# Performance work log

Measured on AMD Instinct MI355X. Metric: run time of the kernel, lower is better.

Reference implementation:

```python
import jax, jax.numpy as jnp
import numpy as np

LAMBDA_POS = 0.5
LAMBDA_RAD = 0.5
LAMBDA_UNPAIR = 0.5
EPS = 1e-6
N_PRED = 20


def setup_inputs() -> dict:
    key = jax.random.key(0)
    k1, k2 = jax.random.split(key)
    B, L = 1000000, 12
    pred = jax.random.uniform(k1, (B, N_PRED, 4), dtype=jnp.float32)
    label = jax.random.uniform(k2, (B, L, 4), dtype=jnp.float32)
    return {"pred": pred, "label": label}


def reference(pred, label):
    # pred: [B, 20, 4] (x, y, radius, prob); label: [B, L, 4]
    B, L = label.shape[0], label.shape[1]
    yl = label[:, :, None, :]   # [B, L, 1, 4]
    yp = pred[:, None, :, :]    # [B, 1, 20, 4]
    dist = jnp.sqrt((yl[..., 0] - yp[..., 0]) ** 2 + (yl[..., 1] - yp[..., 1]) ** 2)  # [B, L, 20]
    rdiff = jnp.abs(yl[..., 2] - yp[..., 2])  # [B, L, 20]
    cost = LAMBDA_POS * dist + LAMBDA_RAD * rdiff  # [B, L, 20]
    idx = jnp.argmin(cost, axis=-1)  # [B, L]

    matched = jnp.take_along_axis(pred, idx[:, :, None], axis=1)  # [B, L, 4]
    mdist = jnp.sqrt((label[..., 0] - matched[..., 0]) ** 2 + (label[..., 1] - matched[..., 1]) ** 2)
    mrdiff = jnp.abs(label[..., 2] - matched[..., 2])
    prob_pair = -jnp.log(matched[..., 3] + EPS)  # prob_loss(p, 1)
    loss_pair = jnp.sum(LAMBDA_POS * mdist + LAMBDA_RAD * mrdiff + prob_pair, axis=-1)  # [B]

    # pair_mask[i] = 1 if any label matched pred i
    mask = jnp.zeros((B, N_PRED), dtype=pred.dtype)
    mask = mask.at[jnp.arange(B)[:, None], idx].set(1.0)

    unpair_term = (-jnp.log(1.0 - pred[..., 3] + EPS) + LAMBDA_RAD * pred[..., 2]) * LAMBDA_UNPAIR  # [B, 20]
    loss_unpair = jnp.sum((1.0 - mask) * unpair_term, axis=-1)  # [B]

    return loss_pair / L + loss_unpair / (N_PRED - L)
```

## Files before the change

kernel.cpp:

```cpp
#include <hip/hip_runtime.h>
#include <math.h>

constexpr int NP = 20;
constexpr int NL = 12;

__global__ __launch_bounds__(256) void myloss_kernel(
    const float4* __restrict__ pred,
    const float4* __restrict__ label,
    float* __restrict__ out,
    int B)
{
#pragma clang fp contract(off)
    int b = blockIdx.x * blockDim.x + threadIdx.x;
    if (b >= B) return;

    const float4* p4 = pred  + (size_t)b * NP;
    const float4* l4 = label + (size_t)b * NL;

    float px[NP], py[NP], pr[NP], pq[NP], up[NP];
#pragma unroll
    for (int j = 0; j < NP; ++j) {
        float4 v = p4[j];
        px[j] = v.x; py[j] = v.y; pr[j] = v.z; pq[j] = v.w;
        up[j] = (-logf(1.0f - v.w + 1e-6f) + 0.5f * v.z) * 0.5f;
    }

    float lp = 0.0f;
    unsigned mask = 0u;
    for (int l = 0; l < NL; ++l) {
        float4 lv = l4[l];
        float best = INFINITY;
        float bq = 0.0f;
        unsigned bbit = 0u;
#pragma unroll
        for (int p = 0; p < NP; ++p) {
            float dx = lv.x - px[p];
            float dy = lv.y - py[p];
            float dist = sqrtf(dx * dx + dy * dy);
            float rd = fabsf(lv.z - pr[p]);
            float c = 0.5f * dist + 0.5f * rd;
            bool lt = c < best;
            best = lt ? c : best;
            bq   = lt ? pq[p] : bq;
            bbit = lt ? (1u << p) : bbit;
        }
        lp += best - logf(bq + 1e-6f);
        mask |= bbit;
    }

    float lu = 0.0f;
#pragma unroll
    for (int p = 0; p < NP; ++p) {
        lu += (mask & (1u << p)) ? 0.0f : up[p];
    }

    out[b] = lp / 12.0f + lu / 8.0f;
}

extern "C" void kernel_launch(void* const* d_in, const int* in_sizes, int n_in,
                              void* d_out, int out_size, void* d_ws, size_t ws_size,
                              hipStream_t stream) {
    const float4* pred  = (const float4*)d_in[0];
    const float4* label = (const float4*)d_in[1];
    float* out = (float*)d_out;
    int B = out_size;
    int threads = 256;
    int blocks = (B + threads - 1) / threads;
    hipLaunchKernelGGL(myloss_kernel, dim3(blocks), dim3(threads), 0, stream,
                       pred, label, out, B);
}
```

Before: 655.1 us.

## Split argmin into four parallel chains, use fast log, defer unpair term

Splits the 20-wide argmin into four independent min chains that are merged with a tie-preserving tree, which shortens the serial dependency chain. The 0.5 scale is factored out of the cost, and logf is replaced with the hardware log2 intrinsic times ln2. The unpaired-term computation moves after the matching loop so fewer registers stay live, and the label loop is unrolled by 2. These trade some precision in the log and a slightly different rounding of the cost for fewer instructions. The kernel is likely memory-bound, so the gain may be limited.

```diff
diff --git a/kernel.cpp b/kernel.cpp
--- a/kernel.cpp
+++ b/kernel.cpp
@@ -3,6 +3,10 @@
 
 constexpr int NP = 20;
 constexpr int NL = 12;
+
+__device__ __forceinline__ float fast_log(float x) {
+    return __builtin_amdgcn_logf(x) * 0.69314718055994530942f;
+}
 
 __global__ __launch_bounds__(256) void myloss_kernel(
     const float4* __restrict__ pred,
@@ -10,51 +14,74 @@
     float* __restrict__ out,
     int B)
 {
-#pragma clang fp contract(off)
     int b = blockIdx.x * blockDim.x + threadIdx.x;
     if (b >= B) return;
 
     const float4* p4 = pred  + (size_t)b * NP;
     const float4* l4 = label + (size_t)b * NL;
 
-    float px[NP], py[NP], pr[NP], pq[NP], up[NP];
+    float px[NP], py[NP], pr[NP], pq[NP];
 #pragma unroll
     for (int j = 0; j < NP; ++j) {
         float4 v = p4[j];
         px[j] = v.x; py[j] = v.y; pr[j] = v.z; pq[j] = v.w;
-        up[j] = (-logf(1.0f - v.w + 1e-6f) + 0.5f * v.z) * 0.5f;
     }
 
     float lp = 0.0f;
     unsigned mask = 0u;
+#pragma unroll 2
     for (int l = 0; l < NL; ++l) {
         float4 lv = l4[l];
-        float best = INFINITY;
-        float bq = 0.0f;
-        unsigned bbit = 0u;
+        float    bs[4];
+        float    bq[4];
+        unsigned bb[4];
 #pragma unroll
-        for (int p = 0; p < NP; ++p) {
-            float dx = lv.x - px[p];
-            float dy = lv.y - py[p];
-            float dist = sqrtf(dx * dx + dy * dy);
-            float rd = fabsf(lv.z - pr[p]);
-            float c = 0.5f * dist + 0.5f * rd;
-            bool lt = c < best;
-            best = lt ? c : best;
-            bq   = lt ? pq[p] : bq;
-            bbit = lt ? (1u << p) : bbit;
+        for (int c = 0; c < 4; ++c) { bs[c] = INFINITY; bq[c] = 0.0f; bb[c] = 0u; }
+#pragma unroll
+        for (int i = 0; i < 5; ++i) {
+#pragma unroll
+            for (int c = 0; c < 4; ++c) {
+                int p = c * 5 + i;
+                float s;
+                {
+#pragma clang fp contract(off)
+                    float dx = lv.x - px[p];
+                    float dy = lv.y - py[p];
+                    float d2 = dx * dx + dy * dy;
+                    float dist = sqrtf(d2);
+                    s = dist + fabsf(lv.z - pr[p]);
+                }
+                bool lt = s < bs[c];
+                bs[c] = lt ? s : bs[c];
+                bq[c] = lt ? pq[p] : bq[c];
+                bb[c] = lt ? (1u << p) : bb[c];
+            }
         }
-        lp += best - logf(bq + 1e-6f);
-        mask |= bbit;
+        bool m01 = bs[1] < bs[0];
+        float sa = m01 ? bs[1] : bs[0];
+        float qa = m01 ? bq[1] : bq[0];
+        unsigned ba = m01 ? bb[1] : bb[0];
+        bool m23 = bs[3] < bs[2];
+        float sb = m23 ? bs[3] : bs[2];
+        float qb = m23 ? bq[3] : bq[2];
+        unsigned bbm = m23 ? bb[3] : bb[2];
+        bool mf = sb < sa;
+        float sm = mf ? sb : sa;
+        float qm = mf ? qb : qa;
+        unsigned bm = mf ? bbm : ba;
+
+        lp += 0.5f * sm - fast_log(qm + 1e-6f);
+        mask |= bm;
     }
 
     float lu = 0.0f;
 #pragma unroll
     for (int p = 0; p < NP; ++p) {
-        lu += (mask & (1u << p)) ? 0.0f : up[p];
+        float t = (-fast_log(1.0f - pq[p] + 1e-6f) + 0.5f * pr[p]) * 0.5f;
+        lu += (mask & (1u << p)) ? 0.0f : t;
     }
 
-    out[b] = lp / 12.0f + lu / 8.0f;
+    out[b] = lp * (1.0f / 12.0f) + lu * 0.125f;
 }
 
 extern "C" void kernel_launch(void* const* d_in, const int* in_sizes, int n_in,
```

Result: faster. 608.5 us (-7.1%).
